# Kernel tuning notes

Measured on AMD Instinct MI355X. Metric: run time of the kernel, lower is better.

Reference implementation:

```python
import jax, jax.numpy as jnp
import numpy as np
from jax import lax

B, C, H, W = 32, 192, 56, 56
HEADS = 8
HD = C // HEADS
SCALE = HD ** -0.5
EPS = 1e-5


def _ln(t, g, b):
    m = jnp.mean(t, axis=-1, keepdims=True)
    v = jnp.mean((t - m) ** 2, axis=-1, keepdims=True)
    return (t - m) / jnp.sqrt(v + EPS) * g + b


def setup_inputs() -> dict:
    ks = jax.random.split(jax.random.key(0), 8)
    x = jax.random.normal(ks[0], (B, C, H, W), jnp.float32)
    bn_gamma = jnp.ones((C,), jnp.float32)
    bn_beta = jnp.zeros((C,), jnp.float32)
    bn_mean = jax.random.normal(ks[1], (C,), jnp.float32) * 0.1
    bn_var = jax.random.uniform(ks[2], (C,), jnp.float32) + 0.5
    conv_w = jax.random.normal(ks[3], (C, 1, 7, 7), jnp.float32) * 0.02  # depthwise, groups=C
    conv_b = jnp.zeros((C,), jnp.float32)
    qkv_w = jax.random.normal(ks[4], (3 * C, C), jnp.float32) * 0.02
    qkv_b = jnp.zeros((3 * C,), jnp.float32)
    ln0_g = jnp.ones((C,), jnp.float32); ln0_b = jnp.zeros((C,), jnp.float32)
    ln1_g = jnp.ones((C,), jnp.float32); ln1_b = jnp.zeros((C,), jnp.float32)
    return {"x": x, "bn_gamma": bn_gamma, "bn_beta": bn_beta, "bn_mean": bn_mean,
            "bn_var": bn_var, "conv_w": conv_w, "conv_b": conv_b,
            "qkv_w": qkv_w, "qkv_b": qkv_b,
            "ln0_g": ln0_g, "ln0_b": ln0_b, "ln1_g": ln1_g, "ln1_b": ln1_b}


def reference(x, bn_gamma, bn_beta, bn_mean, bn_var, conv_w, conv_b,
              qkv_w, qkv_b, ln0_g, ln0_b, ln1_g, ln1_b):
    Bx, Cx, Hx, Wx = x.shape
    N = Hx * Wx
    Bw = Bx * N // 4  # number of 2x2 windows

    # --- window partition: [B,C,H,W] -> [B*N/4, 4, C]
    windows = x.reshape(Bx, Cx, Hx // 2, 2, Wx // 2, 2)
    windows = windows.transpose(0, 2, 4, 3, 5, 1).reshape(Bw, 4, Cx)

    # --- guide-token generator: BN(inference) -> GELU -> depthwise 7x7 s2 conv
    xb = (x - bn_mean[:, None, None]) / jnp.sqrt(bn_var[:, None, None] + EPS)
    xb = xb * bn_gamma[:, None, None] + bn_beta[:, None, None]
    xg = jax.nn.gelu(xb, approximate=False)
    g = lax.conv_general_dilated(xg, conv_w, window_strides=(2, 2),
                                 padding=[(3, 3), (3, 3)],
                                 feature_group_count=Cx,
                                 dimension_numbers=("NCHW", "OIHW", "NCHW"))
    g = g + conv_b[None, :, None, None]              # [B,C,H/2,W/2]
    guide = g.reshape(Bx, Cx, N // 4).transpose(0, 2, 1).reshape(Bw, 1, Cx)

    # --- 5-token windows: guide + 4 local tokens
    tok = jnp.concatenate([guide, windows], axis=1)  # [Bw,5,C]
    t = _ln(tok, ln0_g, ln0_b)

    # --- tiny attention over 5 tokens
    qkv = t @ qkv_w.T + qkv_b                        # [Bw,5,3C]
    qkv = qkv.reshape(Bw, 5, 3, HEADS, HD).transpose(2, 0, 3, 1, 4)  # [3,Bw,h,5,hd]
    q, k, v = qkv[0], qkv[1], qkv[2]
    attn = jax.nn.softmax(jnp.einsum("bhqd,bhkd->bhqk", q, k) * SCALE, axis=-1)
    o = jnp.einsum("bhqk,bhkd->bhqd", attn, v)       # [Bw,h,5,hd]
    o = o.transpose(0, 2, 1, 3).reshape(Bw, 5, Cx)

    out = o[:, 0].reshape(Bx, Hx // 2, Wx // 2, Cx)
    return _ln(out, ln1_g, ln1_b)
```

## Files before the change

kernel.cpp:

```cpp
#include <hip/hip_runtime.h>
#include <hip/hip_bf16.h>
#include <cmath>

#define B_    32
#define C_    192
#define H_    56
#define W_    56
#define EPS_  1e-5f
#define SCALE_ 0.20412414523193154f

using bf = __hip_bfloat16;
typedef __attribute__((ext_vector_type(8))) short short8;
typedef __attribute__((ext_vector_type(4))) float f32x4;

__global__ void k_wconv(const float* __restrict__ qkv_w, bf* __restrict__ wbf) {
    int i = blockIdx.x * 256 + threadIdx.x;
    if (i < 576 * 192) wbf[i] = __float2bfloat16(qkv_w[i]);
}

__global__ __launch_bounds__(256) void k_act_ptok(
        const float* __restrict__ x,
        const float* __restrict__ ln0g, const float* __restrict__ ln0b,
        bf* __restrict__ ptok) {
    __shared__ float tile[C_ * 57];
    __shared__ float mv[W_], rv[W_];
    int b = blockIdx.x / H_, h = blockIdx.x % H_;
    const size_t xbase = ((size_t)b * C_ * H_ + h) * W_;

    for (int i = threadIdx.x; i < C_ * 14; i += 256) {
        int c = i / 14, j = i % 14;
        float4 v = *(const float4*)(x + xbase + (size_t)c * (H_ * W_) + j * 4);
        float* dst = &tile[c * 57 + j * 4];
        dst[0] = v.x; dst[1] = v.y; dst[2] = v.z; dst[3] = v.w;
    }
    __syncthreads();
    if (threadIdx.x < 224) {
        int p = threadIdx.x >> 2, q = threadIdx.x & 3;
        float S = 0.f, Q = 0.f;
        #pragma unroll 8
        for (int j = 0; j < 48; j++) {
            float v = tile[(q * 48 + j) * 57 + p];
            S += v; Q += v * v;
        }
        S += __shfl_xor(S, 1); Q += __shfl_xor(Q, 1);
        S += __shfl_xor(S, 2); Q += __shfl_xor(Q, 2);
        if (q == 0) {
            float mean = S * (1.f / 192.f);
            float var  = Q * (1.f / 192.f) - mean * mean;
            mv[p] = mean; rv[p] = rsqrtf(var + EPS_);
        }
    }
    __syncthreads();
    const size_t pbase = (((size_t)b * H_ + h) * W_) * C_;
    for (int it = threadIdx.x; it < 24 * W_; it += 256) {
        int p = it % W_, cb = it / W_;
        float m = mv[p], r = rv[p];
        bf v8[8];
        #pragma unroll
        for (int e = 0; e < 8; e++) {
            int c = cb * 8 + e;
            v8[e] = __float2bfloat16((tile[c * 57 + p] - m) * r * ln0g[c] + ln0b[c]);
        }
        *(uint4*)(ptok + pbase + (size_t)p * C_ + cb * 8) = *(const uint4*)v8;
    }
}

__global__ __launch_bounds__(256) void k_conv(
        const float* __restrict__ x,
        const float* __restrict__ bn_g, const float* __restrict__ bn_b,
        const float* __restrict__ bn_m, const float* __restrict__ bn_v,
        const float* __restrict__ cw, const float* __restrict__ cb,
        float* __restrict__ gbuf) {
    __shared__ float Apl[4][62][17];
    int tid = threadIdx.x;
    int bc = blockIdx.x;
    int c = bc % C_;

    float* flat = &Apl[0][0][0];
    for (int i = tid; i < 4 * 62 * 17; i += 256) flat[i] = 0.f;
    __syncthreads();

    float bm = bn_m[c];
    float rs = rsqrtf(bn_v[c] + EPS_) * bn_g[c];
    float bb = bn_b[c];
    const float* xp = x + (size_t)bc * (H_ * W_);
    for (int i = tid; i < 784; i += 256) {
        int row = i / 14, j = i % 14;
        float4 v = *(const float4*)(xp + row * W_ + j * 4);
        #pragma unroll
        for (int e = 0; e < 4; e++) {
            float xv = (e == 0) ? v.x : (e == 1) ? v.y : (e == 2) ? v.z : v.w;
            float xn = (xv - bm) * rs + bb;
            float ge = 0.5f * xn * (1.0f + erff(xn * 0.70710678118654752f));
            int pc = 4 * j + 3 + e;
            Apl[pc & 3][row + 3][pc >> 2] = ge;
        }
    }
    __syncthreads();

    float wr[49];
    #pragma unroll
    for (int i = 0; i < 49; i++) wr[i] = cw[c * 49 + i];
    float cbv = cb[c];

    for (int o2 = tid; o2 < 392; o2 += 256) {
        int oh = o2 / 14, g = o2 % 14;
        float acc0 = cbv, acc1 = cbv;
        #pragma unroll
        for (int kh = 0; kh < 7; kh++) {
            int r = 2 * oh + kh;
            float v[9];
            #pragma unroll
            for (int d = 0; d < 9; d++) v[d] = Apl[d & 3][r][g + (d >> 2)];
            #pragma unroll
            for (int kw = 0; kw < 7; kw++) {
                float wv = wr[kh * 7 + kw];
                acc0 += wv * v[kw];
                acc1 += wv * v[kw + 2];
            }
        }
        float2 st = {acc0, acc1};
        *(float2*)(gbuf + (size_t)bc * 784 + oh * 28 + 2 * g) = st;
    }
}

__global__ __launch_bounds__(256) void k_gtok(
        const float* __restrict__ gbuf,
        const float* __restrict__ ln0g, const float* __restrict__ ln0b,
        bf* __restrict__ gtok) {
    __shared__ float tile[C_ * 29];
    __shared__ float mv[28], rv[28];
    int b = blockIdx.x / 28, oh = blockIdx.x % 28;
    size_t gbase = ((size_t)b * C_ * 784) + (size_t)oh * 28;
    for (int i = threadIdx.x; i < C_ * 7; i += 256) {
        int c = i / 7, j = i % 7;
        float4 v = *(const float4*)(gbuf + gbase + (size_t)c * 784 + j * 4);
        float* dst = &tile[c * 29 + j * 4];
        dst[0] = v.x; dst[1] = v.y; dst[2] = v.z; dst[3] = v.w;
    }
    __syncthreads();
    if (threadIdx.x < 112) {
        int p = threadIdx.x >> 2, q = threadIdx.x & 3;
        float S = 0.f, Q = 0.f;
        #pragma unroll 8
        for (int j = 0; j < 48; j++) {
            float v = tile[(q * 48 + j) * 29 + p];
            S += v; Q += v * v;
        }
        S += __shfl_xor(S, 1); Q += __shfl_xor(Q, 1);
        S += __shfl_xor(S, 2); Q += __shfl_xor(Q, 2);
        if (q == 0) {
            float mean = S * (1.f / 192.f);
            float var  = Q * (1.f / 192.f) - mean * mean;
            mv[p] = mean; rv[p] = rsqrtf(var + EPS_);
        }
    }
    __syncthreads();
    size_t tbase = ((size_t)b * 784 + (size_t)oh * 28) * C_;
    for (int it = threadIdx.x; it < 24 * 28; it += 256) {
        int p = it % 28, cb = it / 28;
        float m = mv[p], r = rv[p];
        bf v8[8];
        #pragma unroll
        for (int e = 0; e < 8; e++) {
            int c = cb * 8 + e;
            v8[e] = __float2bfloat16((tile[c * 29 + p] - m) * r * ln0g[c] + ln0b[c]);
        }
        *(uint4*)(gtok + tbase + (size_t)p * C_ + cb * 8) = *(const uint4*)v8;
    }
}

template<int COLOFS, bool WINDOWED>
__global__ __launch_bounds__(256) void k_gemm(
        const bf* __restrict__ A, const bf* __restrict__ wbf,
        const float* __restrict__ qkv_b, bf* __restrict__ out) {
    __shared__ unsigned char Asm_[128 * 384];
    int tid = threadIdx.x;
    size_t r0 = (size_t)blockIdx.x * 128;

    for (int i = tid; i < 128 * 24; i += 256) {
        int row = i / 24, j = i % 24;
        uint4 v = *(const uint4*)((const unsigned char*)(A + (r0 + row) * C_) + j * 16);
        *(uint4*)(Asm_ + row * 384 + ((j * 16) ^ ((row & 7) << 4))) = v;
    }
    __syncthreads();

    int wid = tid >> 6, lane = tid & 63, lo = lane & 15, hi = lane >> 4;
    int xorv = (lo & 7) << 4;
    constexpr int NT = (576 - COLOFS) / 16;

    int dstb[8][4];
    #pragma unroll
    for (int m = 0; m < 8; m++) {
        #pragma unroll
        for (int r = 0; r < 4; r++) {
            int row = m * 16 + hi * 4 + r;
            if (WINDOWED) {
                int p = (int)r0 + row;
                int b = p / 3136, rem = p - b * 3136;
                int h = rem / 56, w = rem - h * 56;
                int bw = b * 784 + (h >> 1) * 28 + (w >> 1);
                int t = (h & 1) * 2 + (w & 1);
                dstb[m][r] = (bw * 4 + t) * 384;
            } else {
                dstb[m][r] = ((int)r0 + row) * (576 - COLOFS);
            }
        }
    }

    for (int nt = wid; nt < NT; nt += 4) {
        int col = COLOFS + nt * 16 + lo;
        float bias = qkv_b[col];
        f32x4 acc[8];
        #pragma unroll
        for (int m = 0; m < 8; m++) acc[m] = {bias, bias, bias, bias};
        const unsigned char* bbase = (const unsigned char*)wbf + (size_t)col * 384 + hi * 16;
        #pragma unroll
        for (int ks = 0; ks < 6; ks++) {
            short8 bfrag = *(const short8*)(bbase + ks * 64);
            int kb = (ks * 64 + hi * 16) ^ xorv;
            #pragma unroll
            for (int m = 0; m < 8; m++) {
                short8 a = *(const short8*)(Asm_ + (m * 16 + lo) * 384 + kb);
                acc[m] = __builtin_amdgcn_mfma_f32_16x16x32_bf16(a, bfrag, acc[m], 0, 0, 0);
            }
        }
        int cofs = col - COLOFS;
        #pragma unroll
        for (int m = 0; m < 8; m++) {
            #pragma unroll
            for (int r = 0; r < 4; r++)
                out[(size_t)dstb[m][r] + cofs] = __float2bfloat16(acc[m][r]);
        }
    }
}

__global__ __launch_bounds__(256) void k_att2(
        const bf* __restrict__ kvp2, const bf* __restrict__ qkvg,
        const float* __restrict__ ln1g, const float* __restrict__ ln1b,
        float* __restrict__ out) {
    int tg = blockIdx.x * 256 + threadIdx.x;
    int bw = tg >> 3, hh = tg & 7;

    const bf* qb = qkvg + (size_t)bw * 576 + hh * 24;
    float q[24];
    #pragma unroll
    for (int j = 0; j < 3; j++) {
        short8 v = *(const short8*)(qb + j * 8);
        #pragma unroll
        for (int e = 0; e < 8; e++)
            q[j * 8 + e] = __uint_as_float(((unsigned)(unsigned short)v[e]) << 16);
    }

    float s[5];
    {
        float a = 0.f;
        #pragma unroll
        for (int j = 0; j < 3; j++) {
            short8 v = *(const short8*)(qb + 192 + j * 8);
            #pragma unroll
            for (int e = 0; e < 8; e++)
                a += q[j * 8 + e] * __uint_as_float(((unsigned)(unsigned short)v[e]) << 16);
        }
        s[0] = a * SCALE_;
    }
    #pragma unroll
    for (int t = 0; t < 4; t++) {
        const bf* kb = kvp2 + ((size_t)bw * 4 + t) * 384 + hh * 24;
        float a = 0.f;
        #pragma unroll
        for (int j = 0; j < 3; j++) {
            short8 v = *(const short8*)(kb + j * 8);
            #pragma unroll
            for (int e = 0; e < 8; e++)
                a += q[j * 8 + e] * __uint_as_float(((unsigned)(unsigned short)v[e]) << 16);
        }
        s[t + 1] = a * SCALE_;
    }
    float mx = fmaxf(fmaxf(fmaxf(s[0], s[1]), fmaxf(s[2], s[3])), s[4]);
    float sum = 0.f;
    #pragma unroll
    for (int t = 0; t < 5; t++) { s[t] = expf(s[t] - mx); sum += s[t]; }
    float inv = 1.f / sum;
    #pragma unroll
    for (int t = 0; t < 5; t++) s[t] *= inv;

    float o[24];
    #pragma unroll
    for (int d = 0; d < 24; d++) o[d] = 0.f;
    {
        #pragma unroll
        for (int j = 0; j < 3; j++) {
            short8 v = *(const short8*)(qb + 384 + j * 8);
            #pragma unroll
            for (int e = 0; e < 8; e++)
                o[j * 8 + e] += s[0] * __uint_as_float(((unsigned)(unsigned short)v[e]) << 16);
        }
    }
    #pragma unroll
    for (int t = 0; t < 4; t++) {
        const bf* vb = kvp2 + ((size_t)bw * 4 + t) * 384 + 192 + hh * 24;
        #pragma unroll
        for (int j = 0; j < 3; j++) {
            short8 v = *(const short8*)(vb + j * 8);
            #pragma unroll
            for (int e = 0; e < 8; e++)
                o[j * 8 + e] += s[t + 1] * __uint_as_float(((unsigned)(unsigned short)v[e]) << 16);
        }
    }

    float S = 0.f, Q = 0.f;
    #pragma unroll
    for (int d = 0; d < 24; d++) { S += o[d]; Q += o[d] * o[d]; }
    S += __shfl_xor(S, 1); Q += __shfl_xor(Q, 1);
    S += __shfl_xor(S, 2); Q += __shfl_xor(Q, 2);
    S += __shfl_xor(S, 4); Q += __shfl_xor(Q, 4);
    float mean = S * (1.f / 192.f);
    float var  = Q * (1.f / 192.f) - mean * mean;
    float rstd = rsqrtf(var + EPS_);
    float* ob = out + (size_t)bw * 192 + hh * 24;
    #pragma unroll
    for (int d = 0; d < 24; d++)
        ob[d] = (o[d] - mean) * rstd * ln1g[hh * 24 + d] + ln1b[hh * 24 + d];
}

extern "C" void kernel_launch(void* const* d_in, const int* in_sizes, int n_in,
                              void* d_out, int out_size, void* d_ws, size_t ws_size,
                              hipStream_t stream) {
    const float* x       = (const float*)d_in[0];
    const float* bn_g    = (const float*)d_in[1];
    const float* bn_b    = (const float*)d_in[2];
    const float* bn_m    = (const float*)d_in[3];
    const float* bn_v    = (const float*)d_in[4];
    const float* conv_w  = (const float*)d_in[5];
    const float* conv_b  = (const float*)d_in[6];
    const float* qkv_w   = (const float*)d_in[7];
    const float* qkv_b   = (const float*)d_in[8];
    const float* ln0g    = (const float*)d_in[9];
    const float* ln0b    = (const float*)d_in[10];
    const float* ln1g    = (const float*)d_in[11];
    const float* ln1b    = (const float*)d_in[12];

    char* ws = (char*)d_ws;
    bf*    ptok = (bf*)(ws);
    bf*    gtok = (bf*)(ws + 38535168);
    bf*    wbf  = (bf*)(ws + 48168960);
    bf*    kvp2 = (bf*)(ws + 48390144);
    bf*    qkvg = (bf*)(ws + 125460480);
    float* gbuf = (float*)(ws + 125460480);

    k_wconv   <<<dim3(432),   dim3(256), 0, stream>>>(qkv_w, wbf);
    k_conv    <<<dim3(B_*C_), dim3(256), 0, stream>>>(x, bn_g, bn_b, bn_m, bn_v,
                                                      conv_w, conv_b, gbuf);
    k_act_ptok<<<dim3(B_*H_), dim3(256), 0, stream>>>(x, ln0g, ln0b, ptok);
    k_gtok    <<<dim3(B_*28), dim3(256), 0, stream>>>(gbuf, ln0g, ln0b, gtok);
    k_gemm<192, true> <<<dim3(784), dim3(256), 0, stream>>>(ptok, wbf, qkv_b, kvp2);
    k_gemm<0, false>  <<<dim3(196), dim3(256), 0, stream>>>(gtok, wbf, qkv_b, qkvg);
    k_att2    <<<dim3(784),  dim3(256), 0, stream>>>(kvp2, qkvg, ln1g, ln1b,
                                                     (float*)d_out);
}
```

Baseline: 322.9 us.

## Fuse LayerNorm into GEMM kernels and fold LN affine into QKV weights

Folds the ln0 gamma/beta into the bf16 QKV weights and bias in a small prep kernel. The per-pixel and guide-token LayerNorm kernels merge into their GEMMs, which now read x/gbuf directly, normalize in shared memory and run MFMA. This removes the ptok/gtok intermediate buffers and two launches. K/V output is stored in pixel order, and the attention kernel computes the window addresses itself. Risks include bf16 rounding before the LN statistics are computed, a single-thread serial loop in weight prep, and smaller GEMM tiles with padded rows.

Measured after the change: 293.0 us. -9.3%, faster.

```diff
diff --git a/kernel.cpp b/kernel.cpp
--- a/kernel.cpp
+++ b/kernel.cpp
@@ -13,56 +13,20 @@
 typedef __attribute__((ext_vector_type(8))) short short8;
 typedef __attribute__((ext_vector_type(4))) float f32x4;
 
-__global__ void k_wconv(const float* __restrict__ qkv_w, bf* __restrict__ wbf) {
-    int i = blockIdx.x * 256 + threadIdx.x;
-    if (i < 576 * 192) wbf[i] = __float2bfloat16(qkv_w[i]);
-}
-
-__global__ __launch_bounds__(256) void k_act_ptok(
-        const float* __restrict__ x,
+__global__ __launch_bounds__(192) void k_wprep(
+        const float* __restrict__ qkv_w, const float* __restrict__ qkv_b,
         const float* __restrict__ ln0g, const float* __restrict__ ln0b,
-        bf* __restrict__ ptok) {
-    __shared__ float tile[C_ * 57];
-    __shared__ float mv[W_], rv[W_];
-    int b = blockIdx.x / H_, h = blockIdx.x % H_;
-    const size_t xbase = ((size_t)b * C_ * H_ + h) * W_;
-
-    for (int i = threadIdx.x; i < C_ * 14; i += 256) {
-        int c = i / 14, j = i % 14;
-        float4 v = *(const float4*)(x + xbase + (size_t)c * (H_ * W_) + j * 4);
-        float* dst = &tile[c * 57 + j * 4];
-        dst[0] = v.x; dst[1] = v.y; dst[2] = v.z; dst[3] = v.w;
-    }
-    __syncthreads();
-    if (threadIdx.x < 224) {
-        int p = threadIdx.x >> 2, q = threadIdx.x & 3;
-        float S = 0.f, Q = 0.f;
-        #pragma unroll 8
-        for (int j = 0; j < 48; j++) {
-            float v = tile[(q * 48 + j) * 57 + p];
-            S += v; Q += v * v;
-        }
-        S += __shfl_xor(S, 1); Q += __shfl_xor(Q, 1);
-        S += __shfl_xor(S, 2); Q += __shfl_xor(Q, 2);
-        if (q == 0) {
-            float mean = S * (1.f / 192.f);
-            float var  = Q * (1.f / 192.f) - mean * mean;
-            mv[p] = mean; rv[p] = rsqrtf(var + EPS_);
-        }
-    }
-    __syncthreads();
-    const size_t pbase = (((size_t)b * H_ + h) * W_) * C_;
-    for (int it = threadIdx.x; it < 24 * W_; it += 256) {
-        int p = it % W_, cb = it / W_;
-        float m = mv[p], r = rv[p];
-        bf v8[8];
-        #pragma unroll
-        for (int e = 0; e < 8; e++) {
-            int c = cb * 8 + e;
-            v8[e] = __float2bfloat16((tile[c * 57 + p] - m) * r * ln0g[c] + ln0b[c]);
-        }
-        *(uint4*)(ptok + pbase + (size_t)p * C_ + cb * 8) = *(const uint4*)v8;
-    }
+        bf* __restrict__ wbf, float* __restrict__ bias2) {
+    int j = blockIdx.x * 192 + threadIdx.x;
+    const float* wr = qkv_w + (size_t)j * 192;
+    bf* wo = wbf + (size_t)j * 192;
+    float acc = 0.f;
+    for (int c = 0; c < 192; c++) {
+        float w = wr[c];
+        acc += w * ln0b[c];
+        wo[c] = __float2bfloat16(w * ln0g[c]);
+    }
+    bias2[j] = qkv_b[j] + acc;
 }
 
 __global__ __launch_bounds__(256) void k_conv(
@@ -124,123 +88,203 @@
     }
 }
 
-__global__ __launch_bounds__(256) void k_gtok(
-        const float* __restrict__ gbuf,
-        const float* __restrict__ ln0g, const float* __restrict__ ln0b,
-        bf* __restrict__ gtok) {
-    __shared__ float tile[C_ * 29];
-    __shared__ float mv[28], rv[28];
-    int b = blockIdx.x / 28, oh = blockIdx.x % 28;
-    size_t gbase = ((size_t)b * C_ * 784) + (size_t)oh * 28;
-    for (int i = threadIdx.x; i < C_ * 7; i += 256) {
-        int c = i / 7, j = i % 7;
-        float4 v = *(const float4*)(gbuf + gbase + (size_t)c * 784 + j * 4);
-        float* dst = &tile[c * 29 + j * 4];
-        dst[0] = v.x; dst[1] = v.y; dst[2] = v.z; dst[3] = v.w;
-    }
-    __syncthreads();
-    if (threadIdx.x < 112) {
-        int p = threadIdx.x >> 2, q = threadIdx.x & 3;
+__global__ __launch_bounds__(256) void k_pgemm(
+        const float* __restrict__ x, const bf* __restrict__ wbf,
+        const float* __restrict__ bias2, bf* __restrict__ kvp) {
+    __shared__ unsigned char Asm_[64 * 384];
+    __shared__ float mv[56], rv[56];
+    int tid = threadIdx.x;
+    int b = blockIdx.x / H_, h = blockIdx.x % H_;
+    const float* xp = x + ((size_t)b * C_ * H_ + h) * W_;
+
+    for (int i = tid; i < 8 * 24; i += 256) {
+        uint4 z = {0u, 0u, 0u, 0u};
+        *(uint4*)(Asm_ + (56 + i / 24) * 384 + (i % 24) * 16) = z;
+    }
+    for (int i = tid; i < C_ * 14; i += 256) {
+        int c = i / 14, j4 = i % 14;
+        float4 v = *(const float4*)(xp + (size_t)c * (H_ * W_) + j4 * 4);
+        #pragma unroll
+        for (int e = 0; e < 4; e++) {
+            int w = j4 * 4 + e;
+            float xv = (e == 0) ? v.x : (e == 1) ? v.y : (e == 2) ? v.z : v.w;
+            *(bf*)(Asm_ + w * 384 + ((2 * c) ^ ((w & 7) << 4))) = __float2bfloat16(xv);
+        }
+    }
+    __syncthreads();
+    if (tid < 224) {
+        int w = tid >> 2, q = tid & 3;
         float S = 0.f, Q = 0.f;
-        #pragma unroll 8
-        for (int j = 0; j < 48; j++) {
-            float v = tile[(q * 48 + j) * 29 + p];
-            S += v; Q += v * v;
+        #pragma unroll
+        for (int jj = 0; jj < 6; jj++) {
+            int j = q * 6 + jj;
+            short8 a = *(const short8*)(Asm_ + w * 384 + ((j * 16) ^ ((w & 7) << 4)));
+            #pragma unroll
+            for (int e = 0; e < 8; e++) {
+                float v = __uint_as_float(((unsigned)(unsigned short)a[e]) << 16);
+                S += v; Q += v * v;
+            }
         }
         S += __shfl_xor(S, 1); Q += __shfl_xor(Q, 1);
         S += __shfl_xor(S, 2); Q += __shfl_xor(Q, 2);
         if (q == 0) {
             float mean = S * (1.f / 192.f);
             float var  = Q * (1.f / 192.f) - mean * mean;
-            mv[p] = mean; rv[p] = rsqrtf(var + EPS_);
-        }
-    }
-    __syncthreads();
-    size_t tbase = ((size_t)b * 784 + (size_t)oh * 28) * C_;
-    for (int it = threadIdx.x; it < 24 * 28; it += 256) {
-        int p = it % 28, cb = it / 28;
-        float m = mv[p], r = rv[p];
-        bf v8[8];
+            mv[w] = mean; rv[w] = rsqrtf(var + EPS_);
+        }
+    }
+    __syncthreads();
+    for (int i = tid; i < 56 * 24; i += 256) {
+        int w = i / 24, j = i % 24;
+        unsigned char* p = Asm_ + w * 384 + ((j * 16) ^ ((w & 7) << 4));
+        short8 a = *(const short8*)p;
+        float m = mv[w], r = rv[w];
+        short8 o;
         #pragma unroll
         for (int e = 0; e < 8; e++) {
-            int c = cb * 8 + e;
-            v8[e] = __float2bfloat16((tile[c * 29 + p] - m) * r * ln0g[c] + ln0b[c]);
-        }
-        *(uint4*)(gtok + tbase + (size_t)p * C_ + cb * 8) = *(const uint4*)v8;
-    }
-}
-
-template<int COLOFS, bool WINDOWED>
-__global__ __launch_bounds__(256) void k_gemm(
-        const bf* __restrict__ A, const bf* __restrict__ wbf,
-        const float* __restrict__ qkv_b, bf* __restrict__ out) {
-    __shared__ unsigned char Asm_[128 * 384];
-    int tid = threadIdx.x;
-    size_t r0 = (size_t)blockIdx.x * 128;
-
-    for (int i = tid; i < 128 * 24; i += 256) {
-        int row = i / 24, j = i % 24;
-        uint4 v = *(const uint4*)((const unsigned char*)(A + (r0 + row) * C_) + j * 16);
-        *(uint4*)(Asm_ + row * 384 + ((j * 16) ^ ((row & 7) << 4))) = v;
-    }
-    __syncthreads();
-
+            float v = __uint_as_float(((unsigned)(unsigned short)a[e]) << 16);
+            bf bv = __float2bfloat16((v - m) * r);
+            o[e] = *(short*)&bv;
+        }
+        *(short8*)p = o;
+    }
+    __syncthreads();
     int wid = tid >> 6, lane = tid & 63, lo = lane & 15, hi = lane >> 4;
     int xorv = (lo & 7) << 4;
-    constexpr int NT = (576 - COLOFS) / 16;
-
-    int dstb[8][4];
-    #pragma unroll
-    for (int m = 0; m < 8; m++) {
-        #pragma unroll
-        for (int r = 0; r < 4; r++) {
-            int row = m * 16 + hi * 4 + r;
-            if (WINDOWED) {
-                int p = (int)r0 + row;
-                int b = p / 3136, rem = p - b * 3136;
-                int h = rem / 56, w = rem - h * 56;
-                int bw = b * 784 + (h >> 1) * 28 + (w >> 1);
-                int t = (h & 1) * 2 + (w & 1);
-                dstb[m][r] = (bw * 4 + t) * 384;
-            } else {
-                dstb[m][r] = ((int)r0 + row) * (576 - COLOFS);
-            }
-        }
-    }
-
-    for (int nt = wid; nt < NT; nt += 4) {
-        int col = COLOFS + nt * 16 + lo;
-        float bias = qkv_b[col];
-        f32x4 acc[8];
-        #pragma unroll
-        for (int m = 0; m < 8; m++) acc[m] = {bias, bias, bias, bias};
+    int pix0 = (b * H_ + h) * W_;
+    for (int nn = 0; nn < 6; nn++) {
+        int nt = nn * 4 + wid;
+        int col = 192 + nt * 16 + lo;
+        float bias = bias2[col];
+        f32x4 acc[4];
+        #pragma unroll
+        for (int m = 0; m < 4; m++) acc[m] = {bias, bias, bias, bias};
         const unsigned char* bbase = (const unsigned char*)wbf + (size_t)col * 384 + hi * 16;
         #pragma unroll
         for (int ks = 0; ks < 6; ks++) {
             short8 bfrag = *(const short8*)(bbase + ks * 64);
             int kb = (ks * 64 + hi * 16) ^ xorv;
             #pragma unroll
-            for (int m = 0; m < 8; m++) {
+            for (int m = 0; m < 4; m++) {
                 short8 a = *(const short8*)(Asm_ + (m * 16 + lo) * 384 + kb);
                 acc[m] = __builtin_amdgcn_mfma_f32_16x16x32_bf16(a, bfrag, acc[m], 0, 0, 0);
             }
         }
-        int cofs = col - COLOFS;
-        #pragma unroll
-        for (int m = 0; m < 8; m++) {
-            #pragma unroll
-            for (int r = 0; r < 4; r++)
-                out[(size_t)dstb[m][r] + cofs] = __float2bfloat16(acc[m][r]);
+        int cofs = col - 192;
+        #pragma unroll
+        for (int m = 0; m < 4; m++) {
+            #pragma unroll
+            for (int r = 0; r < 4; r++) {
+                int row = m * 16 + hi * 4 + r;
+                if (row < 56)
+                    kvp[(size_t)(pix0 + row) * 384 + cofs] = __float2bfloat16(acc[m][r]);
+            }
+        }
+    }
+}
+
+__global__ __launch_bounds__(256) void k_ggemm(
+        const float* __restrict__ gbuf, const bf* __restrict__ wbf,
+        const float* __restrict__ bias2, bf* __restrict__ qkvg) {
+    __shared__ unsigned char Asm_[32 * 384];
+    __shared__ float mv[28], rv[28];
+    int tid = threadIdx.x;
+    int b = blockIdx.x / 28, oh = blockIdx.x % 28;
+    const float* gp = gbuf + (size_t)b * C_ * 784 + (size_t)oh * 28;
+
+    for (int i = tid; i < 4 * 24; i += 256) {
+        uint4 z = {0u, 0u, 0u, 0u};
+        *(uint4*)(Asm_ + (28 + i / 24) * 384 + (i % 24) * 16) = z;
+    }
+    for (int i = tid; i < C_ * 7; i += 256) {
+        int c = i / 7, j4 = i % 7;
+        float4 v = *(const float4*)(gp + (size_t)c * 784 + j4 * 4);
+        #pragma unroll
+        for (int e = 0; e < 4; e++) {
+            int w = j4 * 4 + e;
+            float xv = (e == 0) ? v.x : (e == 1) ? v.y : (e == 2) ? v.z : v.w;
+            *(bf*)(Asm_ + w * 384 + ((2 * c) ^ ((w & 7) << 4))) = __float2bfloat16(xv);
+        }
+    }
+    __syncthreads();
+    if (tid < 112) {
+        int w = tid >> 2, q = tid & 3;
+        float S = 0.f, Q = 0.f;
+        #pragma unroll
+        for (int jj = 0; jj < 6; jj++) {
+            int j = q * 6 + jj;
+            short8 a = *(const short8*)(Asm_ + w * 384 + ((j * 16) ^ ((w & 7) << 4)));
+            #pragma unroll
+            for (int e = 0; e < 8; e++) {
+                float v = __uint_as_float(((unsigned)(unsigned short)a[e]) << 16);
+                S += v; Q += v * v;
+            }
+        }
+        S += __shfl_xor(S, 1); Q += __shfl_xor(Q, 1);
+        S += __shfl_xor(S, 2); Q += __shfl_xor(Q, 2);
+        if (q == 0) {
+            float mean = S * (1.f / 192.f);
+            float var  = Q * (1.f / 192.f) - mean * mean;
+            mv[w] = mean; rv[w] = rsqrtf(var + EPS_);
+        }
+    }
+    __syncthreads();
+    for (int i = tid; i < 28 * 24; i += 256) {
+        int w = i / 24, j = i % 24;
+        unsigned char* p = Asm_ + w * 384 + ((j * 16) ^ ((w & 7) << 4));
+        short8 a = *(const short8*)p;
+        float m = mv[w], r = rv[w];
+        short8 o;
+        #pragma unroll
+        for (int e = 0; e < 8; e++) {
+            float v = __uint_as_float(((unsigned)(unsigned short)a[e]) << 16);
+            bf bv = __float2bfloat16((v - m) * r);
+            o[e] = *(short*)&bv;
+        }
+        *(short8*)p = o;
+    }
+    __syncthreads();
+    int wid = tid >> 6, lane = tid & 63, lo = lane & 15, hi = lane >> 4;
+    int xorv = (lo & 7) << 4;
+    int gpix0 = b * 784 + oh * 28;
+    for (int nn = 0; nn < 9; nn++) {
+        int nt = nn * 4 + wid;
+        int col = nt * 16 + lo;
+        float bias = bias2[col];
+        f32x4 acc[2];
+        #pragma unroll
+        for (int m = 0; m < 2; m++) acc[m] = {bias, bias, bias, bias};
+        const unsigned char* bbase = (const unsigned char*)wbf + (size_t)col * 384 + hi * 16;
+        #pragma unroll
+        for (int ks = 0; ks < 6; ks++) {
+            short8 bfrag = *(const short8*)(bbase + ks * 64);
+            int kb = (ks * 64 + hi * 16) ^ xorv;
+            #pragma unroll
+            for (int m = 0; m < 2; m++) {
+                short8 a = *(const short8*)(Asm_ + (m * 16 + lo) * 384 + kb);
+                acc[m] = __builtin_amdgcn_mfma_f32_16x16x32_bf16(a, bfrag, acc[m], 0, 0, 0);
+            }
+        }
+        #pragma unroll
+        for (int m = 0; m < 2; m++) {
+            #pragma unroll
+            for (int r = 0; r < 4; r++) {
+                int row = m * 16 + hi * 4 + r;
+                if (row < 28)
+                    qkvg[(size_t)(gpix0 + row) * 576 + col] = __float2bfloat16(acc[m][r]);
+            }
         }
     }
 }
 
 __global__ __launch_bounds__(256) void k_att2(
-        const bf* __restrict__ kvp2, const bf* __restrict__ qkvg,
+        const bf* __restrict__ kvp, const bf* __restrict__ qkvg,
         const float* __restrict__ ln1g, const float* __restrict__ ln1b,
         float* __restrict__ out) {
     int tg = blockIdx.x * 256 + threadIdx.x;
     int bw = tg >> 3, hh = tg & 7;
+    int b = bw / 784, rr = bw % 784;
+    int oh = rr / 28, ow = rr % 28;
 
     const bf* qb = qkvg + (size_t)bw * 576 + hh * 24;
     float q[24];
@@ -250,6 +294,12 @@
         #pragma unroll
         for (int e = 0; e < 8; e++)
             q[j * 8 + e] = __uint_as_float(((unsigned)(unsigned short)v[e]) << 16);
+    }
+    size_t pr[4];
+    #pragma unroll
+    for (int t = 0; t < 4; t++) {
+        int h = 2 * oh + (t >> 1), w = 2 * ow + (t & 1);
+        pr[t] = ((size_t)b * H_ + h) * W_ + w;
     }
 
     float s[5];
@@ -266,7 +316,7 @@
     }
     #pragma unroll
     for (int t = 0; t < 4; t++) {
-        const bf* kb = kvp2 + ((size_t)bw * 4 + t) * 384 + hh * 24;
+        const bf* kb = kvp + pr[t] * 384 + hh * 24;
         float a = 0.f;
         #pragma unroll
         for (int j = 0; j < 3; j++) {
@@ -299,7 +349,7 @@
     }
     #pragma unroll
     for (int t = 0; t < 4; t++) {
-        const bf* vb = kvp2 + ((size_t)bw * 4 + t) * 384 + 192 + hh * 24;
+        const bf* vb = kvp + pr[t] * 384 + 192 + hh * 24;
         #pragma unroll
         for (int j = 0; j < 3; j++) {
             short8 v = *(const short8*)(vb + j * 8);
@@ -342,20 +392,17 @@
     const float* ln1b    = (const float*)d_in[12];
 
     char* ws = (char*)d_ws;
-    bf*    ptok = (bf*)(ws);
-    bf*    gtok = (bf*)(ws + 38535168);
-    bf*    wbf  = (bf*)(ws + 48168960);
-    bf*    kvp2 = (bf*)(ws + 48390144);
-    bf*    qkvg = (bf*)(ws + 125460480);
-    float* gbuf = (float*)(ws + 125460480);
-
-    k_wconv   <<<dim3(432),   dim3(256), 0, stream>>>(qkv_w, wbf);
-    k_conv    <<<dim3(B_*C_), dim3(256), 0, stream>>>(x, bn_g, bn_b, bn_m, bn_v,
-                                                      conv_w, conv_b, gbuf);
-    k_act_ptok<<<dim3(B_*H_), dim3(256), 0, stream>>>(x, ln0g, ln0b, ptok);
-    k_gtok    <<<dim3(B_*28), dim3(256), 0, stream>>>(gbuf, ln0g, ln0b, gtok);
-    k_gemm<192, true> <<<dim3(784), dim3(256), 0, stream>>>(ptok, wbf, qkv_b, kvp2);
-    k_gemm<0, false>  <<<dim3(196), dim3(256), 0, stream>>>(gtok, wbf, qkv_b, qkvg);
-    k_att2    <<<dim3(784),  dim3(256), 0, stream>>>(kvp2, qkvg, ln1g, ln1b,
-                                                     (float*)d_out);
-}
+    bf*    wbf   = (bf*)(ws);
+    float* bias2 = (float*)(ws + 221184);
+    float* gbuf  = (float*)(ws + 223488);
+    bf*    kvp   = (bf*)(ws + 19491072);
+    bf*    qkvg  = (bf*)(ws + 96561408);
+
+    k_wprep <<<dim3(3),     dim3(192), 0, stream>>>(qkv_w, qkv_b, ln0g, ln0b, wbf, bias2);
+    k_conv  <<<dim3(B_*C_), dim3(256), 0, stream>>>(x, bn_g, bn_b, bn_m, bn_v,
+                                                    conv_w, conv_b, gbuf);
+    k_pgemm <<<dim3(B_*H_), dim3(256), 0, stream>>>(x, wbf, bias2, kvp);
+    k_ggemm <<<dim3(B_*28), dim3(256), 0, stream>>>(gbuf, wbf, bias2, qkvg);
+    k_att2  <<<dim3(784),   dim3(256), 0, stream>>>(kvp, qkvg, ln1g, ln1b,
+                                                    (float*)d_out);
+}
```
